# Kernel tuning notes

Measured on AMD Instinct MI355X. Metric: run time of the kernel, lower is better.

Reference implementation:

```python
import jax, jax.numpy as jnp
import numpy as np

B, S, E, H = 4, 4096, 1024, 16
D = E // H  # head_dim = 64


def _xavier(key, out_f, in_f):
    lim = float(np.sqrt(6.0 / (in_f + out_f)))
    return jax.random.uniform(key, (out_f, in_f), jnp.float32, -lim, lim)


def setup_inputs() -> dict:
    key = jax.random.key(0)
    ks = jax.random.split(key, 9)
    x = jax.random.normal(ks[0], (B, S, E), jnp.float32)
    Wq = _xavier(ks[1], E, E)
    Wk = _xavier(ks[2], E, E)
    Wv = _xavier(ks[3], E, E)
    Wo = _xavier(ks[4], E, E)
    bq = jnp.zeros((E,), jnp.float32)
    bk = jnp.zeros((E,), jnp.float32)
    bv = jnp.zeros((E,), jnp.float32)
    bo = jnp.zeros((E,), jnp.float32)
    return {"x": x, "Wq": Wq, "bq": bq, "Wk": Wk, "bk": bk,
            "Wv": Wv, "bv": bv, "Wo": Wo, "bo": bo}


def _feature_map(t):
    # elu(t) + 1 (positive feature map)
    return jax.nn.elu(t) + 1.0


def reference(x, Wq, bq, Wk, bk, Wv, bv, Wo, bo):
    b, s, _ = x.shape
    # projections (torch Linear: y = x @ W.T + b), reshape to [b, s, h, d]
    Q = (x @ Wq.T + bq).reshape(b, s, H, D)
    K = (x @ Wk.T + bk).reshape(b, s, H, D)
    V = (x @ Wv.T + bv).reshape(b, s, H, D)
    Q = _feature_map(Q)
    K = _feature_map(K)
    # KV summary: [b, h, d, e]
    KV = jnp.einsum('bshd,bshe->bhde', K, V)
    K_sum = K.sum(axis=1)  # [b, h, d]
    Z = 1.0 / (jnp.einsum('bshd,bhd->bsh', Q, K_sum) + 1e-6)  # [b, s, h]
    out = jnp.einsum('bshd,bhde,bsh->bshe', Q, KV, Z)  # [b, s, h, e]
    out = out.reshape(b, s, E)
    out = out @ Wo.T + bo
    return out
```

## Files before the change

### kernel.cpp

```cpp
#include <hip/hip_runtime.h>
#include <math.h>

#define BB 4
#define SS 4096
#define EE 1024
#define HH 16
#define DD 64
#define MM (BB*SS)

typedef _Float16 f16x8 __attribute__((ext_vector_type(8)));
typedef _Float16 f16x4 __attribute__((ext_vector_type(4)));
typedef float    f32x4 __attribute__((ext_vector_type(4)));

typedef __attribute__((address_space(3))) void lds_void;
typedef __attribute__((address_space(1))) void gm_void;

__device__ __forceinline__ void gload16(const void* g, void* l) {
  __builtin_amdgcn_global_load_lds((gm_void*)g, (lds_void*)l, 16, 0, 0);
}

__global__ __launch_bounds__(256) void conv_x_kernel(const float* __restrict__ x,
                                                     _Float16* __restrict__ xh, int n4) {
  int i = blockIdx.x * blockDim.x + threadIdx.x;
  int stride = gridDim.x * blockDim.x;
  for (; i < n4; i += stride) {
    f32x4 v = *(const f32x4*)&x[(size_t)i * 4];
    f16x4 h;
    h[0] = (_Float16)v[0]; h[1] = (_Float16)v[1];
    h[2] = (_Float16)v[2]; h[3] = (_Float16)v[3];
    *(f16x4*)&xh[(size_t)i * 4] = h;
  }
}

__global__ __launch_bounds__(256) void conv_w_kernel(const float* __restrict__ Wq,
                                                     const float* __restrict__ Wk,
                                                     const float* __restrict__ Wv,
                                                     const float* __restrict__ Wo,
                                                     _Float16* __restrict__ wqkv,
                                                     _Float16* __restrict__ woh) {
  const int per = (EE * EE) / 4;
  int i = blockIdx.x * blockDim.x + threadIdx.x;
  int stride = gridDim.x * blockDim.x;
  for (; i < 4 * per; i += stride) {
    int seg = i / per, off = i - seg * per;
    const float* src = (seg == 0) ? Wq : (seg == 1) ? Wk : (seg == 2) ? Wv : Wo;
    _Float16* dst = (seg < 3) ? (wqkv + (size_t)seg * EE * EE) : woh;
    f32x4 v = *(const f32x4*)&src[(size_t)off * 4];
    f16x4 h;
    h[0] = (_Float16)v[0]; h[1] = (_Float16)v[1];
    h[2] = (_Float16)v[2]; h[3] = (_Float16)v[3];
    *(f16x4*)&dst[(size_t)off * 4] = h;
  }
}


#define SCB() __builtin_amdgcn_sched_barrier(0)
#define VMW4 asm volatile("s_waitcnt vmcnt(4)" ::: "memory")
#define VMW0 asm volatile("s_waitcnt vmcnt(0)" ::: "memory")
#define BARR do { SCB(); __builtin_amdgcn_s_barrier(); SCB(); } while (0)
#define NOP_ do {} while (0)

#define STAGE_A(t, h) gload16(Ag + (size_t)(h) * 262144 + (size_t)(t) * 64,  \
                              LdsA + (((t) & 3) << 14) + ((h) << 13) + wvb)
#define STAGE_B(t, h) gload16(Bg + (size_t)(h) * 262144 + (size_t)(t) * 64,  \
                              LdsB + (((t) & 3) << 14) + ((h) << 13) + wvb)
#define STG4(t2) do { STAGE_A(t2, 0); STAGE_A(t2, 1);                        \
                      STAGE_B(t2, 0); STAGE_B(t2, 1); } while (0)

#define RD_A(bb, mf) (*(const f16x8*)(LdsA + ((bb) << 14) + wrb + ((mf) << 10) + lof))
#define RD_B(bb, nf) (*(const f16x8*)(LdsB + ((bb) << 14) + wcb + ((nf) << 10) + lof))

#define TILE_(t, STG, VW, BAR) do {                                          \
    const int bb = (t) & 3;                                                  \
    f16x8 Bf0 = RD_B(bb, 0), Bf1 = RD_B(bb, 1);                              \
    f16x8 Bf2 = RD_B(bb, 2), Bf3 = RD_B(bb, 3);                              \
    f16x8 Af[8];                                                             \
    _Pragma("unroll") for (int mf = 0; mf < 8; mf++) Af[mf] = RD_A(bb, mf);  \
    STG;                                                                     \
    _Pragma("unroll") for (int mf = 0; mf < 8; mf++) {                       \
      acc[mf][0] = __builtin_amdgcn_mfma_f32_16x16x32_f16(Af[mf], Bf0, acc[mf][0], 0, 0, 0); \
      acc[mf][1] = __builtin_amdgcn_mfma_f32_16x16x32_f16(Af[mf], Bf1, acc[mf][1], 0, 0, 0); \
      acc[mf][2] = __builtin_amdgcn_mfma_f32_16x16x32_f16(Af[mf], Bf2, acc[mf][2], 0, 0, 0); \
      acc[mf][3] = __builtin_amdgcn_mfma_f32_16x16x32_f16(Af[mf], Bf3, acc[mf][3], 0, 0, 0); \
    }                                                                        \
    VW; BAR;                                                                 \
  } while (0)

template <int EPI>
__global__ __launch_bounds__(512, 2) void gemm256(const _Float16* __restrict__ A,
                                                  const _Float16* __restrict__ Bw,
                                                  const float* __restrict__ bias0,
                                                  const float* __restrict__ bias1,
                                                  const float* __restrict__ bias2,
                                                  _Float16* __restrict__ O0,
                                                  _Float16* __restrict__ O1,
                                                  _Float16* __restrict__ O2,
                                                  float* __restrict__ OF) {
  __shared__ __align__(16) char lds[131072];
  char* LdsA = lds;
  char* LdsB = lds + 65536;

  const int tid  = threadIdx.x;
  const int lane = tid & 63;
  const int wv   = tid >> 6;
  const int wr   = wv >> 2;
  const int wc   = wv & 3;
  const int wvb  = wv << 10;
  const int wrb  = wr << 13;
  const int wcb  = wc << 12;

  constexpr int NX = (EPI == 0) ? 12 : 4;
  const int q = (int)gridDim.x >> 3;
  const int bid = (int)blockIdx.x;
  const int sid = (bid & 7) * q + (bid >> 3);
  const int mbase = (sid / NX) << 8;
  const int nbase = (sid % NX) << 8;

  const int lof = ((lane & 15) << 6) + (((lane >> 4) ^ ((lane >> 1) & 3)) << 4);
  const int plane = ((lane >> 2) << 11) + (((lane & 3) ^ ((lane >> 3) & 3)) << 4);

  const char* Ag = (const char*)A + ((size_t)(mbase + wv * 16) << 11) + plane;
  const char* Bg = (const char*)Bw + ((size_t)(nbase + wv * 16) << 11) + plane;

  f32x4 acc[8][4] = {};

  STG4(0); STG4(1);
  VMW4; BARR;

#pragma unroll 1
  for (int i = 0; i < 7; ++i) {
    const int t = i << 2;
    TILE_(t + 0, STG4(t + 2), VMW4, BARR);
    TILE_(t + 1, STG4(t + 3), VMW4, BARR);
    TILE_(t + 2, STG4(t + 4), VMW4, BARR);
    TILE_(t + 3, STG4(t + 5), VMW4, BARR);
  }
  TILE_(28, STG4(30), VMW4, BARR);
  TILE_(29, STG4(31), VMW4, BARR);
  TILE_(30, NOP_, VMW0, BARR);
  TILE_(31, NOP_, NOP_, NOP_);

  const int rl = (lane >> 4) << 2;
  const int cl = lane & 15;
  const int rb = mbase + (wr << 7);
  if (EPI == 0) {
    const int which = nbase >> 10;
    const float* bias = (which == 0) ? bias0 : (which == 1) ? bias1 : bias2;
    _Float16* O = (which == 0) ? O0 : (which == 1) ? O1 : O2;
    const int cb = (nbase & 1023) + (wc << 6);
#pragma unroll
    for (int mf = 0; mf < 8; mf++) {
      const int gm = rb + (mf << 4) + rl;
#pragma unroll
      for (int nf = 0; nf < 4; nf++) {
        const int gc = cb + (nf << 4) + cl;
        const float bz = bias[gc];
#pragma unroll
        for (int j = 0; j < 4; j++) {
          float v = acc[mf][nf][j] + bz;
          if (which < 2) v = (v > 0.f) ? (v + 1.f) : expf(v);
          O[(size_t)(gm + j) * EE + gc] = (_Float16)v;
        }
      }
    }
  } else {
    const int cb = nbase + (wc << 6);
#pragma unroll
    for (int mf = 0; mf < 8; mf++) {
      const int gm = rb + (mf << 4) + rl;
#pragma unroll
      for (int nf = 0; nf < 4; nf++) {
        const int gc = cb + (nf << 4) + cl;
        const float bz = bias0[gc];
#pragma unroll
        for (int j = 0; j < 4; j++)
          OF[(size_t)(gm + j) * EE + gc] = acc[mf][nf][j] + bz;
      }
    }
  }
}

#undef TILE_
#undef RD_A
#undef RD_B
#undef STG4
#undef STAGE_A
#undef STAGE_B

__global__ __launch_bounds__(256) void kv_partial_kernel(const _Float16* __restrict__ Kh,
                                                         const _Float16* __restrict__ Vh,
                                                         float* __restrict__ kvpart,
                                                         float* __restrict__ ksump) {
  __shared__ __align__(16) _Float16 Ks[64 * 64];
  __shared__ __align__(16) _Float16 Vs[64 * 64];
  const int tid = threadIdx.x;
  const int wv = tid >> 6;
  const int bh = blockIdx.x;
  const int chunk = blockIdx.y;
  const int b = bh >> 4, h = bh & 15;
  const int td = tid >> 4, te = tid & 15;
  const int d0 = td * 4, e0 = te * 4;

  float kv[4][4] = {};
  float ks4[4] = {0.f, 0.f, 0.f, 0.f};

  for (int sub = 0; sub < 4; sub++) {
    const int s0 = chunk * 256 + sub * 64;
    __syncthreads();
    {
      const int g0 = tid, g1 = tid + 256;
      gload16((const char*)Kh + ((size_t)(b * SS + s0 + (g0 >> 3)) * EE + h * DD) * 2 + (g0 & 7) * 16,
              (char*)Ks + wv * 1024);
      gload16((const char*)Kh + ((size_t)(b * SS + s0 + (g1 >> 3)) * EE + h * DD) * 2 + (g1 & 7) * 16,
              (char*)Ks + 4096 + wv * 1024);
      gload16((const char*)Vh + ((size_t)(b * SS + s0 + (g0 >> 3)) * EE + h * DD) * 2 + (g0 & 7) * 16,
              (char*)Vs + wv * 1024);
      gload16((const char*)Vh + ((size_t)(b * SS + s0 + (g1 >> 3)) * EE + h * DD) * 2 + (g1 & 7) * 16,
              (char*)Vs + 4096 + wv * 1024);
    }
    __syncthreads();
#pragma unroll 8
    for (int s = 0; s < 64; s++) {
      f16x4 kk = *(const f16x4*)&Ks[s * 64 + d0];
      f16x4 vv = *(const f16x4*)&Vs[s * 64 + e0];
      float kf[4], vf[4];
#pragma unroll
      for (int i = 0; i < 4; i++) { kf[i] = (float)kk[i]; vf[i] = (float)vv[i]; }
#pragma unroll
      for (int i = 0; i < 4; i++)
#pragma unroll
        for (int j = 0; j < 4; j++) kv[i][j] += kf[i] * vf[j];
      if (te == 0) {
#pragma unroll
        for (int i = 0; i < 4; i++) ks4[i] += kf[i];
      }
    }
  }
  const size_t base = ((size_t)chunk * 64 + bh) * 4096;
#pragma unroll
  for (int i = 0; i < 4; i++)
#pragma unroll
    for (int j = 0; j < 4; j++) kvpart[base + (size_t)(d0 + i) * 64 + e0 + j] = kv[i][j];
  if (te == 0) {
#pragma unroll
    for (int i = 0; i < 4; i++) ksump[((size_t)chunk * 64 + bh) * 64 + d0 + i] = ks4[i];
  }
}

__global__ __launch_bounds__(256) void kv_reduce_kernel(const float* __restrict__ kvpart,
                                                        const float* __restrict__ ksump,
                                                        _Float16* __restrict__ kvt,
                                                        float* __restrict__ ksum) {
  const int idx = blockIdx.x * 256 + threadIdx.x;
  if (blockIdx.x < 1024) {
    const int bh = idx >> 12;
    const int rem = idx & 4095;
    float s = 0.f;
#pragma unroll
    for (int c = 0; c < 16; c++) s += kvpart[((size_t)c * 64 + bh) * 4096 + rem];
    const int d = rem >> 6, e = rem & 63;
    kvt[(size_t)bh * 4096 + e * 64 + d] = (_Float16)s;
  } else {
    const int i2 = idx - 1024 * 256;
    const int bh = i2 >> 6, d = i2 & 63;
    float s = 0.f;
#pragma unroll
    for (int c = 0; c < 16; c++) s += ksump[((size_t)c * 64 + bh) * 64 + d];
    ksum[i2] = s;
  }
}

__global__ __launch_bounds__(256) void attn_kernel(const _Float16* __restrict__ Qh,
                                                   const _Float16* __restrict__ kvt,
                                                   const float* __restrict__ ksum,
                                                   _Float16* __restrict__ attn) {
  __shared__ __align__(16) _Float16 Qs[64 * 64];
  __shared__ __align__(16) _Float16 KVs[64 * 64];
  __shared__ float ks_lds[64];
  __shared__ float dpart[4][64];
  __shared__ float zr[64];
  const int tid = threadIdx.x;
  const int lane = tid & 63;
  const int wv = tid >> 6;
  const int stile = blockIdx.x;
  const int bh = blockIdx.y;
  const int b = bh >> 4, h = bh & 15;
  const int m0 = b * SS + stile * 64;

  {
    const int g0 = tid, g1 = tid + 256;
    gload16((const char*)Qh + ((size_t)(m0 + (g0 >> 3)) * EE + h * DD) * 2 + (g0 & 7) * 16,
            (char*)Qs + wv * 1024);
    gload16((const char*)Qh + ((size_t)(m0 + (g1 >> 3)) * EE + h * DD) * 2 + (g1 & 7) * 16,
            (char*)Qs + 4096 + wv * 1024);
    gload16((const char*)kvt + (size_t)bh * 8192 + (size_t)g0 * 16, (char*)KVs + wv * 1024);
    gload16((const char*)kvt + (size_t)bh * 8192 + (size_t)g1 * 16, (char*)KVs + 4096 + wv * 1024);
  }
  if (tid < 64) ks_lds[tid] = ksum[bh * 64 + tid];
  __syncthreads();

  {
    const int r = tid & 63, qd = tid >> 6;
    float p = 0.f;
#pragma unroll
    for (int i = 0; i < 16; i++) p += (float)Qs[r * 64 + qd * 16 + i] * ks_lds[qd * 16 + i];
    dpart[qd][r] = p;
  }
  __syncthreads();
  if (tid < 64) {
    float den = dpart[0][tid] + dpart[1][tid] + dpart[2][tid] + dpart[3][tid];
    zr[tid] = 1.f / (den + 1e-6f);
  }
  __syncthreads();

  f32x4 acc[4] = {};
  const int fr = lane & 15;
  const int kg = (lane >> 4) * 8;
#pragma unroll
  for (int kh = 0; kh < 2; kh++) {
    f16x8 a = *(const f16x8*)&Qs[(wv * 16 + fr) * 64 + kh * 32 + kg];
#pragma unroll
    for (int n = 0; n < 4; n++) {
      f16x8 b8 = *(const f16x8*)&KVs[(n * 16 + fr) * 64 + kh * 32 + kg];
      acc[n] = __builtin_amdgcn_mfma_f32_16x16x32_f16(a, b8, acc[n], 0, 0, 0);
    }
  }

  const int rl = (lane >> 4) * 4, cl = lane & 15;
#pragma unroll
  for (int n = 0; n < 4; n++)
#pragma unroll
    for (int j = 0; j < 4; j++) {
      const int r = wv * 16 + rl + j;
      float v = acc[n][j] * zr[r];
      attn[(size_t)(m0 + r) * EE + h * DD + n * 16 + cl] = (_Float16)v;
    }
}

extern "C" void kernel_launch(void* const* d_in, const int* in_sizes, int n_in,
                              void* d_out, int out_size, void* d_ws, size_t ws_size,
                              hipStream_t stream) {
  const float* x  = (const float*)d_in[0];
  const float* Wq = (const float*)d_in[1];
  const float* bq = (const float*)d_in[2];
  const float* Wk = (const float*)d_in[3];
  const float* bk = (const float*)d_in[4];
  const float* Wv = (const float*)d_in[5];
  const float* bv = (const float*)d_in[6];
  const float* Wo = (const float*)d_in[7];
  const float* bo = (const float*)d_in[8];
  float* out = (float*)d_out;

  char* ws = (char*)d_ws;
  size_t off = 0;
  auto alloc = [&](size_t bytes) -> char* {
    char* p = ws + off;
    off += (bytes + 255) & ~(size_t)255;
    return p;
  };
  _Float16* xh    = (_Float16*)alloc((size_t)MM * EE * 2);
  _Float16* wqkv  = (_Float16*)alloc((size_t)3 * EE * EE * 2);
  _Float16* woh   = (_Float16*)alloc((size_t)EE * EE * 2);
  _Float16* Qh    = (_Float16*)alloc((size_t)MM * EE * 2);
  _Float16* Kh    = (_Float16*)alloc((size_t)MM * EE * 2);
  _Float16* Vh    = (_Float16*)alloc((size_t)MM * EE * 2);
  float*    kvpart= (float*)alloc((size_t)16 * 64 * 4096 * 4);
  float*    ksump = (float*)alloc((size_t)16 * 64 * 64 * 4);
  _Float16* kvt   = (_Float16*)alloc((size_t)64 * 4096 * 2);
  float*    ksum  = (float*)alloc((size_t)64 * 64 * 4);
  _Float16* attn  = xh;

  (void)in_sizes; (void)n_in; (void)out_size; (void)ws_size;

  conv_x_kernel<<<2048, 256, 0, stream>>>(x, xh, (MM * EE) / 4);
  conv_w_kernel<<<1024, 256, 0, stream>>>(Wq, Wk, Wv, Wo, wqkv, woh);
  gemm256<0><<<768, 512, 0, stream>>>(xh, wqkv, bq, bk, bv, Qh, Kh, Vh, nullptr);
  kv_partial_kernel<<<dim3(64, 16), 256, 0, stream>>>(Kh, Vh, kvpart, ksump);
  kv_reduce_kernel<<<1040, 256, 0, stream>>>(kvpart, ksump, kvt, ksum);
  attn_kernel<<<dim3(64, 64), 256, 0, stream>>>(Qh, kvt, ksum, attn);
  gemm256<1><<<256, 512, 0, stream>>>(attn, woh, bo, nullptr, nullptr,
                                      nullptr, nullptr, nullptr, out);
}
```

Before: 261.5 us.

## Double-buffer GEMM LDS fragments in registers and deepen global prefetch

Restructures the GEMM main loop so that fragments for tile t+1 are read from LDS into a second register set while the MFMAs for tile t run. Global-to-LDS prefetch distance grows from two tiles ahead to three, using all four LDS buffers. The MFMA blocks are also wrapped in s_setprio to favour the matrix-issuing waves. The aim is to hide LDS read latency and global load latency behind MFMA work, at the cost of twice the fragment registers, which risks register spills or reduced occupancy under the 512-thread, 2-block launch bounds.

```diff
diff --git a/kernel.cpp b/kernel.cpp
--- a/kernel.cpp
+++ b/kernel.cpp
@@ -70,19 +70,30 @@
 #define RD_A(bb, mf) (*(const f16x8*)(LdsA + ((bb) << 14) + wrb + ((mf) << 10) + lof))
 #define RD_B(bb, nf) (*(const f16x8*)(LdsB + ((bb) << 14) + wcb + ((nf) << 10) + lof))
 
-#define TILE_(t, STG, VW, BAR) do {                                          \
-    const int bb = (t) & 3;                                                  \
-    f16x8 Bf0 = RD_B(bb, 0), Bf1 = RD_B(bb, 1);                              \
-    f16x8 Bf2 = RD_B(bb, 2), Bf3 = RD_B(bb, 3);                              \
-    f16x8 Af[8];                                                             \
-    _Pragma("unroll") for (int mf = 0; mf < 8; mf++) Af[mf] = RD_A(bb, mf);  \
+#define RDF(t_, fA_, fB_) do {                                               \
+    const int bb_ = (t_) & 3;                                                \
+    fB_[0] = RD_B(bb_, 0); fB_[1] = RD_B(bb_, 1);                            \
+    fB_[2] = RD_B(bb_, 2); fB_[3] = RD_B(bb_, 3);                            \
+    _Pragma("unroll") for (int mf_ = 0; mf_ < 8; mf_++)                      \
+      fA_[mf_] = RD_A(bb_, mf_);                                             \
+  } while (0)
+
+#define MFM(fA_, fB_) do {                                                   \
+    __builtin_amdgcn_s_setprio(1);                                           \
+    _Pragma("unroll") for (int mf_ = 0; mf_ < 8; mf_++) {                    \
+      acc[mf_][0] = __builtin_amdgcn_mfma_f32_16x16x32_f16(fA_[mf_], fB_[0], acc[mf_][0], 0, 0, 0); \
+      acc[mf_][1] = __builtin_amdgcn_mfma_f32_16x16x32_f16(fA_[mf_], fB_[1], acc[mf_][1], 0, 0, 0); \
+      acc[mf_][2] = __builtin_amdgcn_mfma_f32_16x16x32_f16(fA_[mf_], fB_[2], acc[mf_][2], 0, 0, 0); \
+      acc[mf_][3] = __builtin_amdgcn_mfma_f32_16x16x32_f16(fA_[mf_], fB_[3], acc[mf_][3], 0, 0, 0); \
+    }                                                                        \
+    __builtin_amdgcn_s_setprio(0);                                           \
+  } while (0)
+
+#define TILEP(t_, fAc, fBc, fAn, fBn, STG, VW, BAR) do {                     \
     STG;                                                                     \
-    _Pragma("unroll") for (int mf = 0; mf < 8; mf++) {                       \
-      acc[mf][0] = __builtin_amdgcn_mfma_f32_16x16x32_f16(Af[mf], Bf0, acc[mf][0], 0, 0, 0); \
-      acc[mf][1] = __builtin_amdgcn_mfma_f32_16x16x32_f16(Af[mf], Bf1, acc[mf][1], 0, 0, 0); \
-      acc[mf][2] = __builtin_amdgcn_mfma_f32_16x16x32_f16(Af[mf], Bf2, acc[mf][2], 0, 0, 0); \
-      acc[mf][3] = __builtin_amdgcn_mfma_f32_16x16x32_f16(Af[mf], Bf3, acc[mf][3], 0, 0, 0); \
-    }                                                                        \
+    RDF((t_) + 1, fAn, fBn);                                                 \
+    SCB();                                                                   \
+    MFM(fAc, fBc);                                                           \
     VW; BAR;                                                                 \
   } while (0)
 
@@ -123,22 +134,25 @@
   const char* Bg = (const char*)Bw + ((size_t)(nbase + wv * 16) << 11) + plane;
 
   f32x4 acc[8][4] = {};
-
-  STG4(0); STG4(1);
+  f16x8 fA0[8], fB0[4];
+  f16x8 fA1[8], fB1[4];
+
+  STG4(0); STG4(1); STG4(2);
   VMW4; BARR;
+  RDF(0, fA0, fB0);
 
 #pragma unroll 1
   for (int i = 0; i < 7; ++i) {
     const int t = i << 2;
-    TILE_(t + 0, STG4(t + 2), VMW4, BARR);
-    TILE_(t + 1, STG4(t + 3), VMW4, BARR);
-    TILE_(t + 2, STG4(t + 4), VMW4, BARR);
-    TILE_(t + 3, STG4(t + 5), VMW4, BARR);
-  }
-  TILE_(28, STG4(30), VMW4, BARR);
-  TILE_(29, STG4(31), VMW4, BARR);
-  TILE_(30, NOP_, VMW0, BARR);
-  TILE_(31, NOP_, NOP_, NOP_);
+    TILEP(t + 0, fA0, fB0, fA1, fB1, STG4(t + 3), VMW4, BARR);
+    TILEP(t + 1, fA1, fB1, fA0, fB0, STG4(t + 4), VMW4, BARR);
+    TILEP(t + 2, fA0, fB0, fA1, fB1, STG4(t + 5), VMW4, BARR);
+    TILEP(t + 3, fA1, fB1, fA0, fB0, STG4(t + 6), VMW4, BARR);
+  }
+  TILEP(28, fA0, fB0, fA1, fB1, STG4(31), VMW4, BARR);
+  TILEP(29, fA1, fB1, fA0, fB0, NOP_,     VMW0, BARR);
+  TILEP(30, fA0, fB0, fA1, fB1, NOP_,     NOP_, NOP_);
+  MFM(fA1, fB1);
 
   const int rl = (lane >> 4) << 2;
   const int cl = lane & 15;
@@ -180,7 +194,9 @@
   }
 }
 
-#undef TILE_
+#undef TILEP
+#undef MFM
+#undef RDF
 #undef RD_A
 #undef RD_B
 #undef STG4
```

After: 275.8 us. 5.5% more time.

## Software-pipeline GEMM LDS fragment reads with register double buffering and deeper prefetch

Applied to the files above, without the earlier changes.

The fp16 MFMA GEMM main loop is restructured so the next tile's B and low-A fragments are read from LDS into a second register set while the current tile's MFMAs run. Each tile's MFMA block is split into two halves, with the high-A reads issued between them. Global-to-LDS prefetch depth grows from two stages to three within the existing four-buffer ring, and MFMA blocks are wrapped in s_setprio. The goal is to hide LDS read latency and global load latency behind matrix math, at the cost of more registers and tighter scheduling constraints.

```diff
diff --git a/kernel.cpp b/kernel.cpp
--- a/kernel.cpp
+++ b/kernel.cpp
@@ -70,19 +70,34 @@
 #define RD_A(bb, mf) (*(const f16x8*)(LdsA + ((bb) << 14) + wrb + ((mf) << 10) + lof))
 #define RD_B(bb, nf) (*(const f16x8*)(LdsB + ((bb) << 14) + wcb + ((nf) << 10) + lof))
 
-#define TILE_(t, STG, VW, BAR) do {                                          \
-    const int bb = (t) & 3;                                                  \
-    f16x8 Bf0 = RD_B(bb, 0), Bf1 = RD_B(bb, 1);                              \
-    f16x8 Bf2 = RD_B(bb, 2), Bf3 = RD_B(bb, 3);                              \
-    f16x8 Af[8];                                                             \
-    _Pragma("unroll") for (int mf = 0; mf < 8; mf++) Af[mf] = RD_A(bb, mf);  \
-    STG;                                                                     \
-    _Pragma("unroll") for (int mf = 0; mf < 8; mf++) {                       \
-      acc[mf][0] = __builtin_amdgcn_mfma_f32_16x16x32_f16(Af[mf], Bf0, acc[mf][0], 0, 0, 0); \
-      acc[mf][1] = __builtin_amdgcn_mfma_f32_16x16x32_f16(Af[mf], Bf1, acc[mf][1], 0, 0, 0); \
-      acc[mf][2] = __builtin_amdgcn_mfma_f32_16x16x32_f16(Af[mf], Bf2, acc[mf][2], 0, 0, 0); \
-      acc[mf][3] = __builtin_amdgcn_mfma_f32_16x16x32_f16(Af[mf], Bf3, acc[mf][3], 0, 0, 0); \
+#define RD4B(t_, dst) do { const int bb_ = (t_) & 3;                         \
+    dst[0] = RD_B(bb_, 0); dst[1] = RD_B(bb_, 1);                            \
+    dst[2] = RD_B(bb_, 2); dst[3] = RD_B(bb_, 3); } while (0)
+#define RD4AL(t_, dst) do { const int bb_ = (t_) & 3;                        \
+    dst[0] = RD_A(bb_, 0); dst[1] = RD_A(bb_, 1);                            \
+    dst[2] = RD_A(bb_, 2); dst[3] = RD_A(bb_, 3); } while (0)
+#define RD4AH(t_, dst) do { const int bb_ = (t_) & 3;                        \
+    dst[0] = RD_A(bb_, 4); dst[1] = RD_A(bb_, 5);                            \
+    dst[2] = RD_A(bb_, 6); dst[3] = RD_A(bb_, 7); } while (0)
+
+#define MFMH(fA_, fB_, MO) do {                                              \
+    __builtin_amdgcn_s_setprio(1);                                           \
+    _Pragma("unroll") for (int mf_ = 0; mf_ < 4; mf_++) {                    \
+      acc[(MO) + mf_][0] = __builtin_amdgcn_mfma_f32_16x16x32_f16(fA_[mf_], fB_[0], acc[(MO) + mf_][0], 0, 0, 0); \
+      acc[(MO) + mf_][1] = __builtin_amdgcn_mfma_f32_16x16x32_f16(fA_[mf_], fB_[1], acc[(MO) + mf_][1], 0, 0, 0); \
+      acc[(MO) + mf_][2] = __builtin_amdgcn_mfma_f32_16x16x32_f16(fA_[mf_], fB_[2], acc[(MO) + mf_][2], 0, 0, 0); \
+      acc[(MO) + mf_][3] = __builtin_amdgcn_mfma_f32_16x16x32_f16(fA_[mf_], fB_[3], acc[(MO) + mf_][3], 0, 0, 0); \
     }                                                                        \
+    __builtin_amdgcn_s_setprio(0);                                           \
+  } while (0)
+
+#define TILEP(t_, fBc, fAc, fBn, fAn, STG, VW, BAR) do {                     \
+    STG; SCB();                                                              \
+    RD4AH(t_, fAhi); SCB();                                                  \
+    MFMH(fAc, fBc, 0);                                                       \
+    SCB();                                                                   \
+    RD4B((t_) + 1, fBn); RD4AL((t_) + 1, fAn); SCB();                        \
+    MFMH(fAhi, fBc, 4);                                                      \
     VW; BAR;                                                                 \
   } while (0)
 
@@ -123,22 +138,28 @@
   const char* Bg = (const char*)Bw + ((size_t)(nbase + wv * 16) << 11) + plane;
 
   f32x4 acc[8][4] = {};
-
-  STG4(0); STG4(1);
+  f16x8 fB0[4], fAlo0[4];
+  f16x8 fB1[4], fAlo1[4];
+  f16x8 fAhi[4];
+
+  STG4(0); STG4(1); STG4(2);
   VMW4; BARR;
+  RD4B(0, fB0); RD4AL(0, fAlo0);
 
 #pragma unroll 1
   for (int i = 0; i < 7; ++i) {
     const int t = i << 2;
-    TILE_(t + 0, STG4(t + 2), VMW4, BARR);
-    TILE_(t + 1, STG4(t + 3), VMW4, BARR);
-    TILE_(t + 2, STG4(t + 4), VMW4, BARR);
-    TILE_(t + 3, STG4(t + 5), VMW4, BARR);
-  }
-  TILE_(28, STG4(30), VMW4, BARR);
-  TILE_(29, STG4(31), VMW4, BARR);
-  TILE_(30, NOP_, VMW0, BARR);
-  TILE_(31, NOP_, NOP_, NOP_);
+    TILEP(t + 0, fB0, fAlo0, fB1, fAlo1, STG4(t + 3), VMW4, BARR);
+    TILEP(t + 1, fB1, fAlo1, fB0, fAlo0, STG4(t + 4), VMW4, BARR);
+    TILEP(t + 2, fB0, fAlo0, fB1, fAlo1, STG4(t + 5), VMW4, BARR);
+    TILEP(t + 3, fB1, fAlo1, fB0, fAlo0, STG4(t + 6), VMW4, BARR);
+  }
+  TILEP(28, fB0, fAlo0, fB1, fAlo1, STG4(31), VMW4, BARR);
+  TILEP(29, fB1, fAlo1, fB0, fAlo0, NOP_,     VMW0, BARR);
+  TILEP(30, fB0, fAlo0, fB1, fAlo1, NOP_,     NOP_, NOP_);
+  RD4AH(31, fAhi); SCB();
+  MFMH(fAlo1, fB1, 0);
+  MFMH(fAhi, fB1, 4);
 
   const int rl = (lane >> 4) << 2;
   const int cl = lane & 15;
@@ -180,7 +201,11 @@
   }
 }
 
-#undef TILE_
+#undef TILEP
+#undef MFMH
+#undef RD4B
+#undef RD4AL
+#undef RD4AH
 #undef RD_A
 #undef RD_B
 #undef STG4
```

Measured after the change: 263.3 us. About the same (+0.7%).

## Retile GEMM to 256x128 tiles with double-buffered LDS and merge conversion kernels

Applied to the files above, without the earlier changes.

The GEMM moves from 512-thread blocks with 256x256 tiles and a 4-stage LDS ring to 256-thread blocks with 256x128 tiles and a 2-stage double buffer using 48KB LDS. The goal is three blocks per CU, for better occupancy and more blocks to cover the grid. It also adds s_setprio around the MFMA section. The two fp32-to-fp16 conversion kernels are merged into one launch. In exchange, the shallower prefetch with a full vmcnt(0) wait every k-step may expose memory latency, and the narrower N tile lowers reuse of A.

```diff
diff --git a/kernel.cpp b/kernel.cpp
--- a/kernel.cpp
+++ b/kernel.cpp
@@ -19,32 +19,31 @@
   __builtin_amdgcn_global_load_lds((gm_void*)g, (lds_void*)l, 16, 0, 0);
 }
 
-__global__ __launch_bounds__(256) void conv_x_kernel(const float* __restrict__ x,
-                                                     _Float16* __restrict__ xh, int n4) {
+__global__ __launch_bounds__(256) void conv_all_kernel(const float* __restrict__ x,
+                                                       const float* __restrict__ Wq,
+                                                       const float* __restrict__ Wk,
+                                                       const float* __restrict__ Wv,
+                                                       const float* __restrict__ Wo,
+                                                       _Float16* __restrict__ xh,
+                                                       _Float16* __restrict__ wqkv,
+                                                       _Float16* __restrict__ woh) {
+  const int nx4 = (MM * EE) / 4;
+  const int per = (EE * EE) / 4;
+  const int ntot = nx4 + 4 * per;
   int i = blockIdx.x * blockDim.x + threadIdx.x;
   int stride = gridDim.x * blockDim.x;
-  for (; i < n4; i += stride) {
-    f32x4 v = *(const f32x4*)&x[(size_t)i * 4];
-    f16x4 h;
-    h[0] = (_Float16)v[0]; h[1] = (_Float16)v[1];
-    h[2] = (_Float16)v[2]; h[3] = (_Float16)v[3];
-    *(f16x4*)&xh[(size_t)i * 4] = h;
-  }
-}
-
-__global__ __launch_bounds__(256) void conv_w_kernel(const float* __restrict__ Wq,
-                                                     const float* __restrict__ Wk,
-                                                     const float* __restrict__ Wv,
-                                                     const float* __restrict__ Wo,
-                                                     _Float16* __restrict__ wqkv,
-                                                     _Float16* __restrict__ woh) {
-  const int per = (EE * EE) / 4;
-  int i = blockIdx.x * blockDim.x + threadIdx.x;
-  int stride = gridDim.x * blockDim.x;
-  for (; i < 4 * per; i += stride) {
-    int seg = i / per, off = i - seg * per;
-    const float* src = (seg == 0) ? Wq : (seg == 1) ? Wk : (seg == 2) ? Wv : Wo;
-    _Float16* dst = (seg < 3) ? (wqkv + (size_t)seg * EE * EE) : woh;
+  for (; i < ntot; i += stride) {
+    const float* src;
+    _Float16* dst;
+    int off;
+    if (i < nx4) {
+      src = x; dst = xh; off = i;
+    } else {
+      int j = i - nx4;
+      int seg = j / per; off = j - seg * per;
+      src = (seg == 0) ? Wq : (seg == 1) ? Wk : (seg == 2) ? Wv : Wo;
+      dst = (seg < 3) ? (wqkv + (size_t)seg * EE * EE) : woh;
+    }
     f32x4 v = *(const f32x4*)&src[(size_t)off * 4];
     f16x4 h;
     h[0] = (_Float16)v[0]; h[1] = (_Float16)v[1];
@@ -55,39 +54,21 @@
 
 
 #define SCB() __builtin_amdgcn_sched_barrier(0)
-#define VMW4 asm volatile("s_waitcnt vmcnt(4)" ::: "memory")
 #define VMW0 asm volatile("s_waitcnt vmcnt(0)" ::: "memory")
 #define BARR do { SCB(); __builtin_amdgcn_s_barrier(); SCB(); } while (0)
-#define NOP_ do {} while (0)
-
-#define STAGE_A(t, h) gload16(Ag + (size_t)(h) * 262144 + (size_t)(t) * 64,  \
-                              LdsA + (((t) & 3) << 14) + ((h) << 13) + wvb)
-#define STAGE_B(t, h) gload16(Bg + (size_t)(h) * 262144 + (size_t)(t) * 64,  \
-                              LdsB + (((t) & 3) << 14) + ((h) << 13) + wvb)
-#define STG4(t2) do { STAGE_A(t2, 0); STAGE_A(t2, 1);                        \
-                      STAGE_B(t2, 0); STAGE_B(t2, 1); } while (0)
-
-#define RD_A(bb, mf) (*(const f16x8*)(LdsA + ((bb) << 14) + wrb + ((mf) << 10) + lof))
-#define RD_B(bb, nf) (*(const f16x8*)(LdsB + ((bb) << 14) + wcb + ((nf) << 10) + lof))
-
-#define TILE_(t, STG, VW, BAR) do {                                          \
-    const int bb = (t) & 3;                                                  \
-    f16x8 Bf0 = RD_B(bb, 0), Bf1 = RD_B(bb, 1);                              \
-    f16x8 Bf2 = RD_B(bb, 2), Bf3 = RD_B(bb, 3);                              \
-    f16x8 Af[8];                                                             \
-    _Pragma("unroll") for (int mf = 0; mf < 8; mf++) Af[mf] = RD_A(bb, mf);  \
-    STG;                                                                     \
-    _Pragma("unroll") for (int mf = 0; mf < 8; mf++) {                       \
-      acc[mf][0] = __builtin_amdgcn_mfma_f32_16x16x32_f16(Af[mf], Bf0, acc[mf][0], 0, 0, 0); \
-      acc[mf][1] = __builtin_amdgcn_mfma_f32_16x16x32_f16(Af[mf], Bf1, acc[mf][1], 0, 0, 0); \
-      acc[mf][2] = __builtin_amdgcn_mfma_f32_16x16x32_f16(Af[mf], Bf2, acc[mf][2], 0, 0, 0); \
-      acc[mf][3] = __builtin_amdgcn_mfma_f32_16x16x32_f16(Af[mf], Bf3, acc[mf][3], 0, 0, 0); \
-    }                                                                        \
-    VW; BAR;                                                                 \
-  } while (0)
+
+#define STAGE_A(t, g) gload16(Ag + ((size_t)(g) << 15) + (size_t)(t) * 64,   \
+                              LdsA + (((t) & 1) << 14) + (((wv << 2) + (g)) << 10))
+#define STAGE_B(t, g) gload16(Bg + ((size_t)(g) << 15) + (size_t)(t) * 64,   \
+                              LdsB + (((t) & 1) << 13) + (((wv << 1) + (g)) << 10))
+#define STG6(t) do { STAGE_A(t, 0); STAGE_A(t, 1); STAGE_A(t, 2);            \
+                     STAGE_B(t, 0); STAGE_B(t, 1); STAGE_A(t, 3); } while (0)
+
+#define RD_A(par, mf) (*(const f16x8*)(LdsA + ((par) << 14) + ((wr8 + (mf)) << 10) + lof))
+#define RD_B(par, nf) (*(const f16x8*)(LdsB + ((par) << 13) + ((wc4 + (nf)) << 10) + lof))
 
 template <int EPI>
-__global__ __launch_bounds__(512, 2) void gemm256(const _Float16* __restrict__ A,
+__global__ __launch_bounds__(256, 3) void gemm256(const _Float16* __restrict__ A,
                                                   const _Float16* __restrict__ Bw,
                                                   const float* __restrict__ bias0,
                                                   const float* __restrict__ bias1,
@@ -96,49 +77,55 @@
                                                   _Float16* __restrict__ O1,
                                                   _Float16* __restrict__ O2,
                                                   float* __restrict__ OF) {
-  __shared__ __align__(16) char lds[131072];
+  __shared__ __align__(16) char lds[49152];
   char* LdsA = lds;
-  char* LdsB = lds + 65536;
+  char* LdsB = lds + 32768;
 
   const int tid  = threadIdx.x;
   const int lane = tid & 63;
   const int wv   = tid >> 6;
-  const int wr   = wv >> 2;
-  const int wc   = wv & 3;
-  const int wvb  = wv << 10;
-  const int wrb  = wr << 13;
-  const int wcb  = wc << 12;
-
-  constexpr int NX = (EPI == 0) ? 12 : 4;
+  const int wr   = wv >> 1;
+  const int wc   = wv & 1;
+  const int wr8  = wr << 3;
+  const int wc4  = wc << 2;
+
+  constexpr int NXT = (EPI == 0) ? 24 : 8;
   const int q = (int)gridDim.x >> 3;
   const int bid = (int)blockIdx.x;
   const int sid = (bid & 7) * q + (bid >> 3);
-  const int mbase = (sid / NX) << 8;
-  const int nbase = (sid % NX) << 8;
+  const int mbase = (sid / NXT) << 8;
+  const int nbase = (sid % NXT) << 7;
 
   const int lof = ((lane & 15) << 6) + (((lane >> 4) ^ ((lane >> 1) & 3)) << 4);
   const int plane = ((lane >> 2) << 11) + (((lane & 3) ^ ((lane >> 3) & 3)) << 4);
 
-  const char* Ag = (const char*)A + ((size_t)(mbase + wv * 16) << 11) + plane;
-  const char* Bg = (const char*)Bw + ((size_t)(nbase + wv * 16) << 11) + plane;
+  const char* Ag = (const char*)A + ((size_t)(mbase + (wv << 6)) << 11) + plane;
+  const char* Bg = (const char*)Bw + ((size_t)(nbase + (wv << 5)) << 11) + plane;
 
   f32x4 acc[8][4] = {};
 
-  STG4(0); STG4(1);
-  VMW4; BARR;
+  STG6(0);
+  VMW0; BARR;
 
 #pragma unroll 1
-  for (int i = 0; i < 7; ++i) {
-    const int t = i << 2;
-    TILE_(t + 0, STG4(t + 2), VMW4, BARR);
-    TILE_(t + 1, STG4(t + 3), VMW4, BARR);
-    TILE_(t + 2, STG4(t + 4), VMW4, BARR);
-    TILE_(t + 3, STG4(t + 5), VMW4, BARR);
-  }
-  TILE_(28, STG4(30), VMW4, BARR);
-  TILE_(29, STG4(31), VMW4, BARR);
-  TILE_(30, NOP_, VMW0, BARR);
-  TILE_(31, NOP_, NOP_, NOP_);
+  for (int t = 0; t < 32; ++t) {
+    const int par = t & 1;
+    if (t < 31) STG6(t + 1);
+    f16x8 fB0 = RD_B(par, 0), fB1 = RD_B(par, 1);
+    f16x8 fB2 = RD_B(par, 2), fB3 = RD_B(par, 3);
+    __builtin_amdgcn_s_setprio(1);
+#pragma unroll
+    for (int mf = 0; mf < 8; mf++) {
+      if (mf == 4) SCB();
+      f16x8 fA = RD_A(par, mf);
+      acc[mf][0] = __builtin_amdgcn_mfma_f32_16x16x32_f16(fA, fB0, acc[mf][0], 0, 0, 0);
+      acc[mf][1] = __builtin_amdgcn_mfma_f32_16x16x32_f16(fA, fB1, acc[mf][1], 0, 0, 0);
+      acc[mf][2] = __builtin_amdgcn_mfma_f32_16x16x32_f16(fA, fB2, acc[mf][2], 0, 0, 0);
+      acc[mf][3] = __builtin_amdgcn_mfma_f32_16x16x32_f16(fA, fB3, acc[mf][3], 0, 0, 0);
+    }
+    __builtin_amdgcn_s_setprio(0);
+    if (t < 31) { VMW0; BARR; }
+  }
 
   const int rl = (lane >> 4) << 2;
   const int cl = lane & 15;
@@ -180,10 +167,9 @@
   }
 }
 
-#undef TILE_
 #undef RD_A
 #undef RD_B
-#undef STG4
+#undef STG6
 #undef STAGE_A
 #undef STAGE_B
 
@@ -372,12 +358,11 @@
 
   (void)in_sizes; (void)n_in; (void)out_size; (void)ws_size;
 
-  conv_x_kernel<<<2048, 256, 0, stream>>>(x, xh, (MM * EE) / 4);
-  conv_w_kernel<<<1024, 256, 0, stream>>>(Wq, Wk, Wv, Wo, wqkv, woh);
-  gemm256<0><<<768, 512, 0, stream>>>(xh, wqkv, bq, bk, bv, Qh, Kh, Vh, nullptr);
+  conv_all_kernel<<<2560, 256, 0, stream>>>(x, Wq, Wk, Wv, Wo, xh, wqkv, woh);
+  gemm256<0><<<1536, 256, 0, stream>>>(xh, wqkv, bq, bk, bv, Qh, Kh, Vh, nullptr);
   kv_partial_kernel<<<dim3(64, 16), 256, 0, stream>>>(Kh, Vh, kvpart, ksump);
   kv_reduce_kernel<<<1040, 256, 0, stream>>>(kvpart, ksump, kvt, ksum);
   attn_kernel<<<dim3(64, 64), 256, 0, stream>>>(Qh, kvt, ksum, attn);
-  gemm256<1><<<256, 512, 0, stream>>>(attn, woh, bo, nullptr, nullptr,
+  gemm256<1><<<512, 256, 0, stream>>>(attn, woh, bo, nullptr, nullptr,
                                       nullptr, nullptr, nullptr, out);
 }
```

Result: no change. 261.8 us (+0.1%).
